# Kernel optimization log

Hardware: AMD Instinct MI355X
Metric: run time of the kernel (lower is better)

## Reference

```python
import jax, jax.numpy as jnp
from jax import lax
import numpy as np

B, H, W = 8, 96, 96
CIN, COUT, QD, NH = 256, 128, 32, 8
LA_MID = COUT // 8  # 16
GRIDS = (6, 3, 2, 1)
EPS = 1e-5  # torch BatchNorm default eps


def conv2d(x, w):
    # 'same' padding for 3x3 stride 1 (autopad k//2)
    return lax.conv_general_dilated(x, w, (1, 1), 'SAME',
                                    dimension_numbers=('NCHW', 'OIHW', 'NCHW'))


def bn2d(x, g, b, m, v):
    inv = g / jnp.sqrt(v + EPS)
    return x * inv[None, :, None, None] + (b - m * inv)[None, :, None, None]


def adaptive_avg_pool_tokens(x, oh, ow):
    # matches torch adaptive_avg_pool2d bin edges; returns [b, c, oh*ow]
    b, c, h, w = x.shape
    cells = []
    for i in range(oh):
        h0, h1 = (i * h) // oh, -((-(i + 1) * h) // oh)
        for j in range(ow):
            w0, w1 = (j * w) // ow, -((-(j + 1) * w) // ow)
            cells.append(x[:, :, h0:h1, w0:w1].mean(axis=(2, 3)))
    return jnp.stack(cells, axis=-1)


def psp(x, grids):
    b, c, h, w = x.shape
    ar = w / h
    return jnp.concatenate(
        [adaptive_avg_pool_tokens(x, g, max(1, round(ar * g))) for g in grids], axis=2)


def setup_inputs() -> dict:
    key = jax.random.key(0)
    ks = jax.random.split(key, 9)
    f = jnp.float32
    return {
        'x': jax.random.normal(ks[0], (B, CIN, H, W), f),
        'w_red': jax.random.normal(ks[1], (COUT, CIN, 3, 3), f) * 0.02,
        'bng': jnp.ones((COUT,), f), 'bnb': jnp.zeros((COUT,), f),
        'bnm': jnp.zeros((COUT,), f), 'bnv': jnp.ones((COUT,), f),
        'w_q': jax.random.normal(ks[2], (QD, COUT), f) * 0.1,
        'b_q': jnp.zeros((QD,), f),
        'w_k': jax.random.normal(ks[3], (QD, COUT), f) * 0.1,
        'b_k': jnp.zeros((QD,), f),
        'w_v': jax.random.normal(ks[4], (COUT, COUT), f) * 0.08,
        'b_v': jnp.zeros((COUT,), f),
        'lsh': jax.random.normal(ks[5], (NH, QD), f),
        'w_la1': jax.random.normal(ks[6], (LA_MID, COUT), f) * 0.1,
        'lag': jnp.ones((LA_MID,), f), 'lab': jnp.zeros((LA_MID,), f),
        'lam': jnp.zeros((LA_MID,), f), 'lav': jnp.ones((LA_MID,), f),
        'w_la2': jax.random.normal(ks[7], (COUT, LA_MID, 3, 3), f) * 0.02,
    }


def reference(x, w_red, bng, bnb, bnm, bnv, w_q, b_q, w_k, b_k, w_v, b_v,
              lsh, w_la1, lag, lab, lam, lav, w_la2):
    # reduce_channel: Conv(256,128,3) = conv + BN + SiLU
    xr = jax.nn.silu(bn2d(conv2d(x, w_red), bng, bnb, bnm, bnv))  # [B,COUT,H,W]
    b, c, h, w = xr.shape
    # query: 1x1 conv to 32 ch, flatten spatial -> [B, HW, QD]
    q = (jnp.einsum('oc,bchw->bohw', w_q, xr)
         + b_q[None, :, None, None]).reshape(b, QD, h * w).transpose(0, 2, 1)
    # key_psp and value_psp act on the same xr -> identical token sets [B,COUT,50]
    tokens = psp(xr, GRIDS)
    k_tok = (jnp.einsum('oc,bcn->bon', w_k, tokens)
             + b_k[None, :, None]).transpose(0, 2, 1)  # [B,50,QD]
    v_tok = (jnp.einsum('oc,bcn->bon', w_v, tokens)
             + b_v[None, :, None]).transpose(0, 2, 1)  # [B,50,COUT]
    # ReformerAttention: argmax over TOKEN dim -> [B, NH]; sort indices lie in [0,NH)
    # so the gather picks a per-batch permutation of the first NH key/value tokens
    # (faithful to the torch code; q_buckets is computed but unused there).
    k_buckets = jnp.argmax(jnp.einsum('hd,bnd->bhn', lsh, k_tok), axis=-1)  # [B,NH]
    k_idx = jnp.argsort(k_buckets, axis=-1)  # [B,NH], values in [0,NH)
    k_s = jnp.take_along_axis(k_tok, k_idx[:, :, None], axis=1)  # [B,NH,QD]
    v_s = jnp.take_along_axis(v_tok, k_idx[:, :, None], axis=1)  # [B,NH,COUT]
    att = jax.nn.softmax(jnp.einsum('bqd,bkd->bqk', q, k_s), axis=-1)  # [B,HW,NH]
    ctx = jnp.einsum('bqk,bkd->bqd', att, v_s).transpose(0, 2, 1).reshape(b, COUT, h, w)
    # LocalAttenModule: Conv(128,16,1)(conv+bn+silu) -> 3x3 conv 16->128 -> tanh mask
    y = jax.nn.silu(bn2d(jnp.einsum('oc,bchw->bohw', w_la1, ctx), lag, lab, lam, lav))
    mask = jnp.tanh(conv2d(y, w_la2))
    ctx = ctx * mask + ctx
    return xr + ctx
```

## Files before the change

### kernel.cpp

```cpp
#include <hip/hip_runtime.h>
#include <hip/hip_bf16.h>
#include <cmath>

typedef __attribute__((ext_vector_type(8))) short short8;
typedef __attribute__((ext_vector_type(16))) short short16;
typedef __attribute__((ext_vector_type(4))) short s16x4;
typedef __attribute__((ext_vector_type(4))) float f32x4;
typedef __attribute__((ext_vector_type(2))) float f32x2;
typedef unsigned short u16;

#define HW 9216

__device__ inline float bf2f(u16 u) {
    union { unsigned int i; float f; } x; x.i = ((unsigned int)u) << 16; return x.f;
}
__device__ inline u16 f2bf(float f) {
    union { unsigned int i; float f; } x; x.f = f;
    unsigned int r = x.i + 0x7FFF + ((x.i >> 16) & 1);
    return (u16)(r >> 16);
}

__device__ inline void gload16(const u16* g, u16* l) {
    __builtin_amdgcn_global_load_lds(
        (const __attribute__((address_space(1))) void*)g,
        (__attribute__((address_space(3))) void*)l,
        16, 0, 0);
}

#define VWAIT4 asm volatile("s_waitcnt vmcnt(4)" ::: "memory")
#define VWAIT3 asm volatile("s_waitcnt vmcnt(3)" ::: "memory")
#define VWAIT0 asm volatile("s_waitcnt vmcnt(0)" ::: "memory")

__global__ __launch_bounds__(256) void prex_k(
    const float* __restrict__ X, u16* __restrict__ Xt,
    const float* __restrict__ wred, const float* __restrict__ wla2,
    u16* __restrict__ Wt1, u16* __restrict__ Wt2)
{
    __shared__ u16 Lt[256 * 35];
    int t = threadIdx.x;
    int bid = blockIdx.x;
    if (bid < 2304) {
        int b = bid & 7;
        int p0 = (bid >> 3) * 32;
        int pp = t & 31, cg = t >> 5;
        const float* xb = X + (size_t)b * 256 * HW + p0 + pp;
        for (int r = 0; r < 32; ++r) {
            int c = r * 8 + cg;
            Lt[c * 35 + pp] = f2bf(xb[(size_t)c * HW]);
        }
        __syncthreads();
        int p = t >> 3, cq = t & 7;
        u16* ot = Xt + ((size_t)b * HW + p0 + p) * 256 + cq * 32;
#pragma unroll
        for (int o = 0; o < 2; ++o) {
            short16 v;
#pragma unroll
            for (int j = 0; j < 16; ++j)
                v[j] = (short)Lt[(cq * 32 + o * 16 + j) * 35 + p];
            *(short16*)(ot + o * 16) = v;
        }
    } else {
        int idx = (bid - 2304) * 256 + t;
        if (idx < 128 * 2304) {
            int co = idx / 2304;
            int rem = idx - co * 2304;
            int c = rem / 288;
            int r2 = rem - c * 288;
            int khw = r2 >> 5, ciL = r2 & 31;
            Wt1[idx] = f2bf(wred[((co * 256 + c * 32 + ciL) * 9 + khw)]);
        } else {
            int i2 = idx - 128 * 2304;
            if (i2 < 128 * 160) {
                int co = i2 / 160;
                int k = i2 - co * 160;
                int khw = k >> 4, ci = k & 15;
                Wt2[i2] = (khw < 9) ? f2bf(wla2[((co << 4) + ci) * 9 + khw]) : (u16)0;
            }
        }
    }
}

template<int CIN, int KTILES, int KP, int EPI>
__global__ __launch_bounds__(256) void conv_k(
    const u16* __restrict__ Xt, const u16* __restrict__ Wt,
    u16* OutH, float* OutF,
    const float* __restrict__ bg, const float* __restrict__ bb,
    const float* __restrict__ bm, const float* __restrict__ bv,
    const u16* __restrict__ xrb, const float* ctxf,
    const u16* __restrict__ zp)
{
    __shared__ __align__(16) short As[3][128 * 32];
    __shared__ __align__(16) short Bs[3][96 * 32];
    __shared__ float invA[128], betA[128];

    const int tid = threadIdx.x;
    const int bid = blockIdx.x;
    const int b = bid & 7;
    const int tile = bid >> 3;
    const int w0 = (tile % 3) * 32;
    const int h0 = (tile / 3) * 3;

    const int lane = tid & 63;
    const int wid = tid >> 6;
    const int wm = (wid & 1) * 64;
    const int wn = (wid >> 1) * 48;
    const int r = lane & 15;
    const int quad = lane >> 4;

    const u16* XtB = Xt + (size_t)b * HW * CIN;

    auto bsrc = [&](int slot, int kt) -> const u16* {
        int row = slot >> 2, o = slot & 3;
        int pw = row & 31, ph = row >> 5;
        int hgl = h0 + ph, wgl = w0 + pw;
        if (CIN == 256) {
            int c = (kt * 57) >> 9;
            int khw = kt - c * 9;
            int dh = (khw * 11) >> 5;
            int dw = khw - 3 * dh;
            int hh = hgl + dh - 1, ww = wgl + dw - 1;
            bool ok = ((unsigned)hh < 96u) && ((unsigned)ww < 96u);
            return ok ? XtB + ((size_t)hh * 96 + ww) * 256 + c * 32 + o * 8 : zp;
        } else {
            int kg = kt * 32 + o * 8;
            int khw = kg >> 4, ci0 = kg & 15;
            int dh = (khw * 11) >> 5, dw = khw - 3 * dh;
            int hh = hgl + dh - 1, ww = wgl + dw - 1;
            bool ok = ((unsigned)hh < 96u) && ((unsigned)ww < 96u) && (khw < 9);
            return ok ? XtB + ((size_t)hh * 96 + ww) * 16 + ci0 : zp;
        }
    };

    auto stage = [&](int kt, int buf) {
        int sA0 = tid, sA1 = tid + 256;
        gload16(Wt + (size_t)(sA0 >> 2) * KP + kt * 32 + (sA0 & 3) * 8,
                (u16*)&As[buf][(64 * wid) * 8]);
        gload16(Wt + (size_t)(sA1 >> 2) * KP + kt * 32 + (sA1 & 3) * 8,
                (u16*)&As[buf][(256 + 64 * wid) * 8]);
        gload16(bsrc(tid, kt), (u16*)&Bs[buf][(64 * wid) * 8]);
        if (wid < 2)
            gload16(bsrc(tid + 256, kt), (u16*)&Bs[buf][(256 + 64 * wid) * 8]);
    };

    f32x4 acc[4][3];
    f32x4 zz = {0.f, 0.f, 0.f, 0.f};
#pragma unroll
    for (int i = 0; i < 4; i++)
#pragma unroll
        for (int j = 0; j < 3; j++) acc[i][j] = zz;

    stage(0, 0);
    stage(1, 1);
    if (wid < 2) VWAIT4; else VWAIT3;
    __builtin_amdgcn_s_barrier();

    for (int kt = 0; kt < KTILES; ++kt) {
        int cur = kt % 3;
        if (kt + 2 < KTILES) stage(kt + 2, (kt + 2) % 3);
        short8 af[4], bfr[3];
#pragma unroll
        for (int i = 0; i < 4; i++)
            af[i] = *(const short8*)(&As[cur][(wm + i * 16 + r) * 32 + quad * 8]);
#pragma unroll
        for (int j = 0; j < 3; j++)
            bfr[j] = *(const short8*)(&Bs[cur][(wn + j * 16 + r) * 32 + quad * 8]);
        __builtin_amdgcn_s_setprio(1);
#pragma unroll
        for (int i = 0; i < 4; i++)
#pragma unroll
            for (int j = 0; j < 3; j++)
                acc[i][j] = __builtin_amdgcn_mfma_f32_16x16x32_bf16(af[i], bfr[j], acc[i][j], 0, 0, 0);
        __builtin_amdgcn_s_setprio(0);
        if (kt + 1 < KTILES) {
            if (kt + 2 < KTILES) { if (wid < 2) VWAIT4; else VWAIT3; }
            else VWAIT0;
            __builtin_amdgcn_s_barrier();
        }
    }

    if constexpr (EPI == 1) {
        if (tid < 128) {
            float iv = bg[tid] * rsqrtf(bv[tid] + 1e-5f);
            invA[tid] = iv;
            betA[tid] = bb[tid] - bm[tid] * iv;
        }
        __syncthreads();
    }

#pragma unroll
    for (int i = 0; i < 4; i++) {
#pragma unroll
        for (int j = 0; j < 3; j++) {
            int pl = wn + j * 16 + r;
            int w = w0 + (pl & 31), h = h0 + (pl >> 5);
#pragma unroll
            for (int g = 0; g < 4; ++g) {
                int co = wm + i * 16 + quad * 4 + g;
                float v = acc[i][j][g];
                size_t oidx = ((size_t)b * 128 + co) * HW + h * 96 + w;
                if constexpr (EPI == 1) {
                    float val = v * invA[co] + betA[co];
                    float sv = val / (1.f + __expf(-val));
                    OutH[oidx] = f2bf(sv);
                } else {
                    float xv = bf2f(xrb[oidx]);
                    float cv = ctxf[oidx];
                    float e = __expf(2.f * v);
                    float th = 1.f - 2.f / (e + 1.f);
                    OutF[oidx] = xv + cv * (1.f + th);
                }
            }
        }
    }
}

__global__ __launch_bounds__(256) void prep_attn(
    const u16* __restrict__ xr,
    const float* __restrict__ wk, const float* __restrict__ bk,
    const float* __restrict__ wv, const float* __restrict__ bv,
    const float* __restrict__ wq, const float* __restrict__ bq,
    const float* __restrict__ wla1,
    float* __restrict__ Aout, float* __restrict__ Vout, float* __restrict__ c0out,
    float* __restrict__ WVout)
{
    __shared__ float part[256];
    __shared__ float tok[128];
    __shared__ float ks[32];
    __shared__ float vs[128];
    int t = threadIdx.x;
    int bid = blockIdx.x;
    int b = bid & 7, n = bid >> 3;
    int c = t & 127, half = t >> 7;
    int i0 = (n < 6) ? 0 : 16;
    int j0 = ((n < 6) ? n : (n - 6)) * 16;
    const u16* xb = xr + (size_t)(b * 128 + c) * HW;

    float s = 0.f;
    for (int rr = 0; rr < 8; ++rr) {
        int row = i0 + half * 8 + rr;
        const u16* rp = xb + row * 96 + j0;
        short8 v0 = *(const short8*)rp;
        short8 v1 = *(const short8*)(rp + 8);
#pragma unroll
        for (int j = 0; j < 8; ++j) s += bf2f((u16)v0[j]) + bf2f((u16)v1[j]);
    }
    part[t] = s;
    __syncthreads();
    if (t < 128) tok[t] = (part[t] + part[t + 128]) * (1.f / 256.f);
    __syncthreads();
    if (t < 32) {
        float s2 = bk[t];
        for (int cc = 0; cc < 128; ++cc) s2 += wk[t * 128 + cc] * tok[cc];
        ks[t] = s2;
    }
    __syncthreads();
    if (t < 128) {
        float s3 = bv[c];
        for (int c2 = 0; c2 < 128; ++c2) s3 += wv[c * 128 + c2] * tok[c2];
        Vout[((size_t)b * 8 + n) * 128 + c] = s3;
        vs[c] = s3;
    } else {
        float s4 = 0.f;
        for (int d = 0; d < 32; ++d) s4 += wq[d * 128 + c] * ks[d];
        Aout[((size_t)b * 8 + n) * 128 + c] = s4;
    }
    if (t == 0) {
        float s5 = 0.f;
        for (int d = 0; d < 32; ++d) s5 += bq[d] * ks[d];
        c0out[b * 8 + n] = s5;
    }
    __syncthreads();
    if (t < 16) {
        float s6 = 0.f;
        for (int cc = 0; cc < 128; ++cc) s6 += vs[cc] * wla1[t * 128 + cc];
        WVout[((size_t)b * 8 + n) * 16 + t] = s6;
    }
}

__global__ __launch_bounds__(256) void attn_k(
    const u16* __restrict__ xr,
    const float* __restrict__ Ain, const float* __restrict__ Vin,
    const float* __restrict__ c0in, const float* __restrict__ WVin,
    const float* __restrict__ lag, const float* __restrict__ lab,
    const float* __restrict__ lam, const float* __restrict__ lav,
    float* __restrict__ ctxout, u16* __restrict__ yout)
{
    __shared__ __align__(16) u16 Xh[64 * 136];
    __shared__ __align__(16) float Ast[8 * 128];
    __shared__ __align__(16) float Vst[8 * 128];
    __shared__ float WVs[128];
    __shared__ float satt[8 * 64];
    __shared__ float c0s[8], inv1[16], bet1[16];

    int t = threadIdx.x;
    int bid = blockIdx.x;
    int b = bid & 7;
    int p0 = (bid >> 3) * 64;

    for (int i = t; i < 1024; i += 256) {
        Ast[i] = Ain[b * 1024 + i];
        Vst[i] = Vin[b * 1024 + i];
    }
    if (t < 128) WVs[t] = WVin[b * 128 + t];
    if (t < 8) c0s[t] = c0in[b * 8 + t];
    if (t < 16) {
        float iv = lag[t] * rsqrtf(lav[t] + 1e-5f);
        inv1[t] = iv; bet1[t] = lab[t] - lam[t] * iv;
    }
    const u16* xb = xr + (size_t)b * 128 * HW + p0;
#pragma unroll
    for (int it = 0; it < 4; ++it) {
        int c = (t >> 3) + it * 32;
        int seg = t & 7;
        short8 v = *(const short8*)(xb + (size_t)c * HW + seg * 8);
#pragma unroll
        for (int j = 0; j < 8; ++j)
            Xh[(seg * 8 + j) * 136 + c] = (u16)v[j];
    }
    __syncthreads();
    {
        int pp = t & 63, ng = t >> 6;
        const float* A0 = &Ast[(ng * 2) * 128];
        const float* A1 = &Ast[(ng * 2 + 1) * 128];
        const u16* xrow = &Xh[pp * 136];
        float a0 = 0.f, a1 = 0.f;
        for (int c8 = 0; c8 < 16; ++c8) {
            short8 xv = *(const short8*)(&xrow[c8 * 8]);
            f32x4 q00 = *(const f32x4*)(&A0[c8 * 8]);
            f32x4 q01 = *(const f32x4*)(&A0[c8 * 8 + 4]);
            f32x4 q10 = *(const f32x4*)(&A1[c8 * 8]);
            f32x4 q11 = *(const f32x4*)(&A1[c8 * 8 + 4]);
#pragma unroll
            for (int j = 0; j < 4; ++j) {
                float x = bf2f((u16)xv[j]);
                a0 += q00[j] * x; a1 += q10[j] * x;
            }
#pragma unroll
            for (int j = 0; j < 4; ++j) {
                float x = bf2f((u16)xv[j + 4]);
                a0 += q01[j] * x; a1 += q11[j] * x;
            }
        }
        satt[(ng * 2) * 64 + pp] = a0 + c0s[ng * 2];
        satt[(ng * 2 + 1) * 64 + pp] = a1 + c0s[ng * 2 + 1];
    }
    __syncthreads();
    if (t < 64) {
        float m = -1e30f;
        float sv[8];
#pragma unroll
        for (int n = 0; n < 8; ++n) { sv[n] = satt[n * 64 + t]; m = fmaxf(m, sv[n]); }
        float sum = 0.f;
#pragma unroll
        for (int n = 0; n < 8; ++n) { sv[n] = __expf(sv[n] - m); sum += sv[n]; }
        float rcp = 1.f / sum;
#pragma unroll
        for (int n = 0; n < 8; ++n) satt[n * 64 + t] = sv[n] * rcp;
    }
    __syncthreads();
    {
        int pp = t & 63, cg = t >> 6;
        float at[8];
#pragma unroll
        for (int n = 0; n < 8; ++n) at[n] = satt[n * 64 + pp];
        for (int c4 = 0; c4 < 8; ++c4) {
            int c = cg * 32 + c4 * 4;
            float s0 = 0.f, s1 = 0.f, s2 = 0.f, s3 = 0.f;
#pragma unroll
            for (int n = 0; n < 8; ++n) {
                f32x4 vv = *(const f32x4*)(&Vst[n * 128 + c]);
                s0 += at[n] * vv[0]; s1 += at[n] * vv[1];
                s2 += at[n] * vv[2]; s3 += at[n] * vv[3];
            }
            size_t obase = ((size_t)b * 128 + c) * HW + p0 + pp;
            ctxout[obase] = s0;
            ctxout[obase + HW] = s1;
            ctxout[obase + 2 * HW] = s2;
            ctxout[obase + 3 * HW] = s3;
        }
        float a[4] = {0.f, 0.f, 0.f, 0.f};
#pragma unroll
        for (int n = 0; n < 8; ++n) {
            f32x4 wv = *(const f32x4*)(&WVs[n * 16 + cg * 4]);
#pragma unroll
            for (int k = 0; k < 4; ++k) a[k] += at[n] * wv[k];
        }
        s16x4 pk;
#pragma unroll
        for (int k = 0; k < 4; ++k) {
            int d = cg * 4 + k;
            float val = a[k] * inv1[d] + bet1[d];
            float s = val / (1.f + __expf(-val));
            pk[k] = (short)f2bf(s);
        }
        *(s16x4*)(yout + ((size_t)b * HW + p0 + pp) * 16 + cg * 4) = pk;
    }
}

extern "C" void kernel_launch(void* const* d_in, const int* in_sizes, int n_in,
                              void* d_out, int out_size, void* d_ws, size_t ws_size,
                              hipStream_t stream)
{
    const float* x    = (const float*)d_in[0];
    const float* wred = (const float*)d_in[1];
    const float* bng  = (const float*)d_in[2];
    const float* bnb  = (const float*)d_in[3];
    const float* bnm  = (const float*)d_in[4];
    const float* bnv  = (const float*)d_in[5];
    const float* wq   = (const float*)d_in[6];
    const float* bq   = (const float*)d_in[7];
    const float* wk   = (const float*)d_in[8];
    const float* bk   = (const float*)d_in[9];
    const float* wv   = (const float*)d_in[10];
    const float* bv   = (const float*)d_in[11];
    const float* wla1 = (const float*)d_in[13];
    const float* lag  = (const float*)d_in[14];
    const float* lab  = (const float*)d_in[15];
    const float* lam  = (const float*)d_in[16];
    const float* lav  = (const float*)d_in[17];
    const float* wla2 = (const float*)d_in[18];

    char* ws = (char*)d_ws;
    u16*   xr  = (u16*)(ws + 0);
    u16*   yt  = (u16*)(ws + 18874368);
    u16*   Wt1 = (u16*)(ws + 21233664);
    u16*   Wt2 = (u16*)(ws + 21823488);
    float* Ab  = (float*)(ws + 21864448);
    float* Vb  = (float*)(ws + 21897216);
    float* c0b = (float*)(ws + 21929984);
    float* WVb = (float*)(ws + 21930240);
    u16*   xt   = (u16*)d_out;
    float* outp = (float*)d_out;
    const u16* zp = Wt2 + 144;

    prex_k<<<dim3(3536), dim3(256), 0, stream>>>(x, xt, wred, wla2, Wt1, Wt2);

    conv_k<256, 72, 2304, 1><<<dim3(768), dim3(256), 0, stream>>>(
        xt, Wt1, xr, nullptr, bng, bnb, bnm, bnv, nullptr, nullptr, zp);

    prep_attn<<<dim3(64), dim3(256), 0, stream>>>(
        xr, wk, bk, wv, bv, wq, bq, wla1, Ab, Vb, c0b, WVb);

    attn_k<<<dim3(1152), dim3(256), 0, stream>>>(
        xr, Ab, Vb, c0b, WVb, lag, lab, lam, lav, outp, yt);

    conv_k<16, 5, 160, 2><<<dim3(768), dim3(256), 0, stream>>>(
        yt, Wt2, nullptr, outp, nullptr, nullptr, nullptr, nullptr, xr, outp, zp);
}
```

Measured before the change: 276.1 us.

## Switch conv pipeline to double buffering and batch epilogue loads

Reduces the conv kernel's LDS ring from three stages to two and replaces the hand-tuned vmcnt waits with plain __syncthreads, so each iteration prefetches only one tile ahead. It also computes the BN scale/bias before the main loop and, in the tanh epilogue, gathers all residual and context loads per column before computing, to expose more memory parallelism. Cutting LDS may raise occupancy. The cost is a shallower prefetch distance and full barriers that wait on all outstanding loads, which can expose global-load latency.

After: 279.4 us. Within noise of the previous version (+1.2%).

```diff
diff --git a/kernel.cpp b/kernel.cpp
--- a/kernel.cpp
+++ b/kernel.cpp
@@ -26,10 +26,6 @@
         (__attribute__((address_space(3))) void*)l,
         16, 0, 0);
 }
-
-#define VWAIT4 asm volatile("s_waitcnt vmcnt(4)" ::: "memory")
-#define VWAIT3 asm volatile("s_waitcnt vmcnt(3)" ::: "memory")
-#define VWAIT0 asm volatile("s_waitcnt vmcnt(0)" ::: "memory")
 
 __global__ __launch_bounds__(256) void prex_k(
     const float* __restrict__ X, u16* __restrict__ Xt,
@@ -89,8 +85,8 @@
     const u16* __restrict__ xrb, const float* ctxf,
     const u16* __restrict__ zp)
 {
-    __shared__ __align__(16) short As[3][128 * 32];
-    __shared__ __align__(16) short Bs[3][96 * 32];
+    __shared__ __align__(16) short As[2][128 * 32];
+    __shared__ __align__(16) short Bs[2][96 * 32];
     __shared__ float invA[128], betA[128];
 
     const int tid = threadIdx.x;
@@ -106,6 +102,14 @@
     const int wn = (wid >> 1) * 48;
     const int r = lane & 15;
     const int quad = lane >> 4;
+
+    if constexpr (EPI == 1) {
+        if (tid < 128) {
+            float iv = bg[tid] * rsqrtf(bv[tid] + 1e-5f);
+            invA[tid] = iv;
+            betA[tid] = bb[tid] - bm[tid] * iv;
+        }
+    }
 
     const u16* XtB = Xt + (size_t)b * HW * CIN;
 
@@ -150,13 +154,11 @@
         for (int j = 0; j < 3; j++) acc[i][j] = zz;
 
     stage(0, 0);
-    stage(1, 1);
-    if (wid < 2) VWAIT4; else VWAIT3;
-    __builtin_amdgcn_s_barrier();
+    __syncthreads();
 
     for (int kt = 0; kt < KTILES; ++kt) {
-        int cur = kt % 3;
-        if (kt + 2 < KTILES) stage(kt + 2, (kt + 2) % 3);
+        int cur = kt & 1;
+        if (kt + 1 < KTILES) stage(kt + 1, cur ^ 1);
         short8 af[4], bfr[3];
 #pragma unroll
         for (int i = 0; i < 4; i++)
@@ -171,43 +173,54 @@
             for (int j = 0; j < 3; j++)
                 acc[i][j] = __builtin_amdgcn_mfma_f32_16x16x32_bf16(af[i], bfr[j], acc[i][j], 0, 0, 0);
         __builtin_amdgcn_s_setprio(0);
-        if (kt + 1 < KTILES) {
-            if (kt + 2 < KTILES) { if (wid < 2) VWAIT4; else VWAIT3; }
-            else VWAIT0;
-            __builtin_amdgcn_s_barrier();
-        }
+        if (kt + 1 < KTILES)
+            __syncthreads();
     }
 
     if constexpr (EPI == 1) {
-        if (tid < 128) {
-            float iv = bg[tid] * rsqrtf(bv[tid] + 1e-5f);
-            invA[tid] = iv;
-            betA[tid] = bb[tid] - bm[tid] * iv;
-        }
-        __syncthreads();
-    }
-
-#pragma unroll
-    for (int i = 0; i < 4; i++) {
+#pragma unroll
+        for (int i = 0; i < 4; i++) {
+#pragma unroll
+            for (int j = 0; j < 3; j++) {
+                int pl = wn + j * 16 + r;
+                int w = w0 + (pl & 31), h = h0 + (pl >> 5);
+#pragma unroll
+                for (int g = 0; g < 4; ++g) {
+                    int co = wm + i * 16 + quad * 4 + g;
+                    float v = acc[i][j][g];
+                    size_t oidx = ((size_t)b * 128 + co) * HW + h * 96 + w;
+                    float val = v * invA[co] + betA[co];
+                    float sv = val / (1.f + __expf(-val));
+                    OutH[oidx] = f2bf(sv);
+                }
+            }
+        }
+    } else {
 #pragma unroll
         for (int j = 0; j < 3; j++) {
             int pl = wn + j * 16 + r;
             int w = w0 + (pl & 31), h = h0 + (pl >> 5);
-#pragma unroll
-            for (int g = 0; g < 4; ++g) {
-                int co = wm + i * 16 + quad * 4 + g;
-                float v = acc[i][j][g];
-                size_t oidx = ((size_t)b * 128 + co) * HW + h * 96 + w;
-                if constexpr (EPI == 1) {
-                    float val = v * invA[co] + betA[co];
-                    float sv = val / (1.f + __expf(-val));
-                    OutH[oidx] = f2bf(sv);
-                } else {
-                    float xv = bf2f(xrb[oidx]);
-                    float cv = ctxf[oidx];
+            float xv[16], cv[16];
+#pragma unroll
+            for (int i = 0; i < 4; i++) {
+#pragma unroll
+                for (int g = 0; g < 4; ++g) {
+                    int co = wm + i * 16 + quad * 4 + g;
+                    size_t oidx = ((size_t)b * 128 + co) * HW + h * 96 + w;
+                    xv[i * 4 + g] = bf2f(xrb[oidx]);
+                    cv[i * 4 + g] = ctxf[oidx];
+                }
+            }
+#pragma unroll
+            for (int i = 0; i < 4; i++) {
+#pragma unroll
+                for (int g = 0; g < 4; ++g) {
+                    int co = wm + i * 16 + quad * 4 + g;
+                    size_t oidx = ((size_t)b * 128 + co) * HW + h * 96 + w;
+                    float v = acc[i][j][g];
                     float e = __expf(2.f * v);
                     float th = 1.f - 2.f / (e + 1.f);
-                    OutF[oidx] = xv + cv * (1.f + th);
+                    OutF[oidx] = xv[i * 4 + g] + cv[i * 4 + g] * (1.f + th);
                 }
             }
         }
```
